# Kernel tuning notes

Hardware: AMD Instinct MI355X
Metric: run time of the kernel (lower is better)

## Reference

```python
import jax, jax.numpy as jnp
import numpy as np

E = 1024
H = 16
HD = E // H  # 64


def setup_inputs() -> dict:
    key = jax.random.key(0)
    ks = jax.random.split(key, 5)
    x = jax.random.normal(ks[0], (2, 2048, E), dtype=jnp.float32)
    s = 1.0 / np.sqrt(E)
    W_qkv = jax.random.uniform(ks[1], (E, 3 * E), jnp.float32, -s, s)
    b_qkv = jax.random.uniform(ks[2], (3 * E,), jnp.float32, -s, s)
    W_out = jax.random.uniform(ks[3], (E, E), jnp.float32, -s, s)
    b_out = jax.random.uniform(ks[4], (E,), jnp.float32, -s, s)
    return {"x": x, "W_qkv": W_qkv, "b_qkv": b_qkv, "W_out": W_out, "b_out": b_out}


def reference(x, W_qkv, b_qkv, W_out, b_out):
    B, N, _ = x.shape
    scale = HD ** (-0.5)
    qkv = x @ W_qkv + b_qkv                         # [B, N, 3E]
    qkv = qkv.reshape(B, N, H, 3 * HD)              # torch layout: per-head 3*hd chunk
    qkv = qkv.transpose(0, 2, 1, 3)                 # [B, H, N, 3*hd]
    q, k, v = jnp.split(qkv, 3, axis=-1)            # each [B, H, N, hd]
    attn = jnp.einsum('bhqd,bhkd->bhqk', q, k) * scale
    attn = jax.nn.softmax(attn, axis=-1)            # dropout is identity in eval
    out = jnp.einsum('bhqk,bhkd->bhqd', attn, v)    # [B, H, N, hd]
    out = out.transpose(0, 2, 1, 3).reshape(B, N, E)
    return out @ W_out + b_out
```

## Files before the change

### kernel.cpp

```cpp
#include <hip/hip_runtime.h>


#define SEQ 2048
#define NH  16

typedef __attribute__((ext_vector_type(8))) short short8;
typedef __attribute__((ext_vector_type(4))) short short4v;
typedef __attribute__((ext_vector_type(4))) float floatx4;
typedef __attribute__((ext_vector_type(4))) _Float16 half4;
typedef __attribute__((ext_vector_type(8))) _Float16 half8;
typedef __attribute__((ext_vector_type(2))) _Float16 half2v;
typedef __attribute__((ext_vector_type(2))) __fp16 fp16x2;

#define QSCALE 0.1803368801111204f

__device__ __forceinline__ short f2bf(float f) {
    union { float f; unsigned u; } v; v.f = f;
    unsigned r = v.u + 0x7fffu + ((v.u >> 16) & 1u);
    return (short)(r >> 16);
}

__device__ __forceinline__ float fast_exp2(float x) {
#if __has_builtin(__builtin_amdgcn_exp2f)
    return __builtin_amdgcn_exp2f(x);
#else
    return exp2f(x);
#endif
}

__device__ __forceinline__ half2v cvt_pk(float a, float b) {
#if __has_builtin(__builtin_amdgcn_cvt_pkrtz)
    union { fp16x2 i; half2v o; } u;
    u.i = __builtin_amdgcn_cvt_pkrtz(a, b);
    return u.o;
#else
    half2v r; r.x = (_Float16)a; r.y = (_Float16)b; return r;
#endif
}

#define GLDS16(gp, lp)                                                          \
    __builtin_amdgcn_global_load_lds(                                           \
        (const __attribute__((address_space(1))) unsigned int*)(gp),            \
        (__attribute__((address_space(3))) unsigned int*)(lp), 16, 0, 0)

__global__ __launch_bounds__(256) void prep_kernel(
    const float* __restrict__ x,  short* __restrict__ xb,
    const float* __restrict__ wq, short* __restrict__ wqkvt,
    const float* __restrict__ wo, short* __restrict__ woutt)
{
    const int tid = threadIdx.x;
    const int b = blockIdx.x;
    if (b < 2048) {
        int i = b * 256 + tid;
        const float4* in4 = (const float4*)x + (size_t)i * 2;
        float4 a = in4[0], c = in4[1];
        short8 o = { f2bf(a.x), f2bf(a.y), f2bf(a.z), f2bf(a.w),
                     f2bf(c.x), f2bf(c.y), f2bf(c.z), f2bf(c.w) };
        *((short8*)xb + i) = o;
        return;
    }
    __shared__ float T[64][65];
    const float* in; short* out; int R, C, c0, r0;
    if (b < 2816) {
        int t = b - 2048; in = wq; out = wqkvt; R = 1024; C = 3072;
        c0 = (t % 48) * 64; r0 = (t / 48) * 64;
    } else {
        int t = b - 2816; in = wo; out = woutt; R = 1024; C = 1024;
        c0 = (t & 15) * 64; r0 = (t >> 4) * 64;
    }
#pragma unroll
    for (int it = 0; it < 4; ++it) {
        int r = it * 16 + (tid >> 4), c = (tid & 15) * 4;
        float4 v = *(const float4*)(in + (size_t)(r0 + r) * C + c0 + c);
        T[c+0][r] = v.x; T[c+1][r] = v.y; T[c+2][r] = v.z; T[c+3][r] = v.w;
    }
    __syncthreads();
#pragma unroll
    for (int it = 0; it < 4; ++it) {
        int oc = it * 16 + (tid >> 4), k = (tid & 15) * 4;
        short4v o = { f2bf(T[oc][k]), f2bf(T[oc][k+1]), f2bf(T[oc][k+2]), f2bf(T[oc][k+3]) };
        *(short4v*)(out + (size_t)(c0 + oc) * R + r0 + k) = o;
    }
}

__global__ __launch_bounds__(256) void vtrans_kernel(
    const _Float16* __restrict__ vn, _Float16* __restrict__ vt)
{
    __shared__ _Float16 T[64][72];
    const int tid = threadIdx.x;
    const int bh = blockIdx.y, n0 = blockIdx.x * 64;
#pragma unroll
    for (int it = 0; it < 2; ++it) {
        int n = it * 32 + (tid >> 3), c = (tid & 7) * 8;
        const _Float16* p = vn + ((size_t)bh * SEQ + n0 + n) * 64 + c;
        half4 a = *(const half4*)(p);
        half4 b = *(const half4*)(p + 4);
        T[c+0][n] = a.x; T[c+1][n] = a.y; T[c+2][n] = a.z; T[c+3][n] = a.w;
        T[c+4][n] = b.x; T[c+5][n] = b.y; T[c+6][n] = b.z; T[c+7][n] = b.w;
    }
    __syncthreads();
#pragma unroll
    for (int it = 0; it < 2; ++it) {
        int idx = it * 256 + tid;
        int quad = idx & 3, d = (idx >> 2) & 63, u = idx >> 8;
        const _Float16* row = &T[d][u * 32 + quad * 4];
        half4 lo = *(const half4*)(row);
        half4 hi = *(const half4*)(row + 16);
        _Float16* q = vt + ((size_t)bh * 64 + d) * SEQ + n0 + u * 32 + quad * 8;
        *(half4*)(q)     = lo;
        *(half4*)(q + 4) = hi;
    }
}

#define GEMM_CORE(A_PTR, B_PTR, LDA, LDB)                                        \
    __shared__ short As[128 * 32];                                               \
    __shared__ short Bs[128 * 32];                                               \
    const int tid  = threadIdx.x;                                                \
    const int lane = tid & 63, w = tid >> 6;                                     \
    const int quad = lane >> 4, l16 = lane & 15;                                 \
    const int wm = w >> 1, wn = w & 1;                                           \
    const int c0 = blockIdx.x * 128, r0 = blockIdx.y * 128;                      \
    floatx4 acc[4][4];                                                           \
    _Pragma("unroll")                                                            \
    for (int i = 0; i < 4; ++i)                                                  \
        _Pragma("unroll")                                                        \
        for (int j = 0; j < 4; ++j) acc[i][j] = (floatx4){0.f, 0.f, 0.f, 0.f};   \
    const int srow = tid >> 2;                                                   \
    const int sgx  = ((tid & 3) ^ ((srow >> 1) & 3)) * 8;                        \
    const short* Ag = (A_PTR) + (size_t)(r0 + srow) * (LDA) + sgx;               \
    const short* Bg = (B_PTR) + (size_t)(c0 + srow) * (LDB) + sgx;               \
    const int fsw = (l16 >> 1) & 3;                                              \
    for (int kk = 0; kk < 1024; kk += 32) {                                      \
        __syncthreads();                                                         \
        GLDS16(Ag + kk,                      As + tid * 8);                      \
        GLDS16(Ag + (size_t)64 * (LDA) + kk, As + 2048 + tid * 8);               \
        GLDS16(Bg + kk,                      Bs + tid * 8);                      \
        GLDS16(Bg + (size_t)64 * (LDB) + kk, Bs + 2048 + tid * 8);               \
        __syncthreads();                                                         \
        short8 af[4], bf[4];                                                     \
        _Pragma("unroll")                                                        \
        for (int mt = 0; mt < 4; ++mt)                                           \
            af[mt] = *(const short8*)&As[(wm * 64 + mt * 16 + l16) * 32 + (quad ^ fsw) * 8]; \
        _Pragma("unroll")                                                        \
        for (int nt = 0; nt < 4; ++nt)                                           \
            bf[nt] = *(const short8*)&Bs[(wn * 64 + nt * 16 + l16) * 32 + (quad ^ fsw) * 8]; \
        _Pragma("unroll")                                                        \
        for (int mt = 0; mt < 4; ++mt)                                           \
            _Pragma("unroll")                                                    \
            for (int nt = 0; nt < 4; ++nt)                                       \
                acc[mt][nt] = __builtin_amdgcn_mfma_f32_16x16x32_bf16(           \
                    af[mt], bf[nt], acc[mt][nt], 0, 0, 0);                       \
    }

__global__ __launch_bounds__(256) void qkv_gemm_kernel(
    const short* __restrict__ wt, const short* __restrict__ xb,
    const float* __restrict__ bias,
    short* __restrict__ qb, short* __restrict__ kb, _Float16* __restrict__ vnb)
{
    GEMM_CORE(wt, xb, 1024, 1024)
#pragma unroll
    for (int mt = 0; mt < 4; ++mt) {
        int oc0 = r0 + wm * 64 + mt * 16 + quad * 4;
        int head = oc0 / 192;
        int t = (oc0 - head * 192) >> 6;
        int d0 = oc0 & 63;
        float4 bv = *(const float4*)(bias + oc0);
#pragma unroll
        for (int nt = 0; nt < 4; ++nt) {
            int tok = c0 + wn * 64 + nt * 16 + l16;
            int bh = (tok >> 11) * NH + head;
            size_t base = ((size_t)bh * SEQ + (tok & (SEQ - 1))) * 64 + d0;
            float v0 = acc[mt][nt][0] + bv.x, v1 = acc[mt][nt][1] + bv.y;
            float v2 = acc[mt][nt][2] + bv.z, v3 = acc[mt][nt][3] + bv.w;
            if (t == 0) {
                short4v o = { f2bf(v0 * QSCALE), f2bf(v1 * QSCALE),
                              f2bf(v2 * QSCALE), f2bf(v3 * QSCALE) };
                *(short4v*)(qb + base) = o;
            } else if (t == 1) {
                short4v o = { f2bf(v0), f2bf(v1), f2bf(v2), f2bf(v3) };
                *(short4v*)(kb + base) = o;
            } else {
                half4 o = { (_Float16)v0, (_Float16)v1, (_Float16)v2, (_Float16)v3 };
                *(half4*)(vnb + base) = o;
            }
        }
    }
}

__global__ __launch_bounds__(512) void out_gemm_kernel(
    const short* __restrict__ wt, const short* __restrict__ ab,
    const float* __restrict__ bias, float* __restrict__ out)
{
    __shared__ short As[128 * 32];
    __shared__ short Bs[128 * 32];
    const int tid  = threadIdx.x;
    const int lane = tid & 63, w = tid >> 6;
    const int quad = lane >> 4, l16 = lane & 15;
    const int wm = w >> 2, wn = w & 3;
    const int c0 = blockIdx.x * 128, r0 = blockIdx.y * 128;
    floatx4 acc[4][2];
#pragma unroll
    for (int i = 0; i < 4; ++i)
#pragma unroll
        for (int j = 0; j < 2; ++j) acc[i][j] = (floatx4){0.f, 0.f, 0.f, 0.f};
    const int srow = tid >> 2;
    const int sgx  = ((tid & 3) ^ ((srow >> 1) & 3)) * 8;
    const short* Ag = wt + (size_t)(r0 + srow) * 1024 + sgx;
    const short* Bg = ab + (size_t)(c0 + srow) * 1024 + sgx;
    const int fsw = (l16 >> 1) & 3;
    for (int kk = 0; kk < 1024; kk += 32) {
        __syncthreads();
        GLDS16(Ag + kk, As + tid * 8);
        GLDS16(Bg + kk, Bs + tid * 8);
        __syncthreads();
        short8 af[4], bf[2];
#pragma unroll
        for (int mt = 0; mt < 4; ++mt)
            af[mt] = *(const short8*)&As[(wm * 64 + mt * 16 + l16) * 32 + (quad ^ fsw) * 8];
#pragma unroll
        for (int nt = 0; nt < 2; ++nt)
            bf[nt] = *(const short8*)&Bs[(wn * 32 + nt * 16 + l16) * 32 + (quad ^ fsw) * 8];
#pragma unroll
        for (int mt = 0; mt < 4; ++mt)
#pragma unroll
            for (int nt = 0; nt < 2; ++nt)
                acc[mt][nt] = __builtin_amdgcn_mfma_f32_16x16x32_bf16(
                    af[mt], bf[nt], acc[mt][nt], 0, 0, 0);
    }
#pragma unroll
    for (int mt = 0; mt < 4; ++mt) {
        int oc0 = r0 + wm * 64 + mt * 16 + quad * 4;
        float4 bv = *(const float4*)(bias + oc0);
#pragma unroll
        for (int nt = 0; nt < 2; ++nt) {
            int tok = c0 + wn * 32 + nt * 16 + l16;
            float4 o = { acc[mt][nt][0] + bv.x, acc[mt][nt][1] + bv.y,
                         acc[mt][nt][2] + bv.z, acc[mt][nt][3] + bv.w };
            *(float4*)(out + (size_t)tok * 1024 + oc0) = o;
        }
    }
}

__global__ __launch_bounds__(256, 4) void attn_kernel(
    const short* __restrict__ qb, const short* __restrict__ kb,
    const _Float16* __restrict__ vtb, short* __restrict__ ob)
{
    __shared__ short    Ks[128 * 64];
    __shared__ _Float16 Vts[64 * 128];
    __shared__ float    Ls[4][32];
    const int tid  = threadIdx.x;
    const int lane = tid & 63, w = tid >> 6;
    const int quad = lane >> 4, l16 = lane & 15;
    const int qh = w >> 1, kq = w & 1;
    const int bh = blockIdx.y;
    const int q0 = blockIdx.x * 64;

    short8 aq[2][2];
#pragma unroll
    for (int qf = 0; qf < 2; ++qf) {
        const short* qp = qb + ((size_t)bh * SEQ + q0 + qh * 32 + qf * 16 + l16) * 64 + quad * 8;
        aq[qf][0] = *(const short8*)(qp);
        aq[qf][1] = *(const short8*)(qp + 32);
    }

    const int krow = tid >> 3, kg = tid & 7;
    const short* kgp = kb + ((size_t)bh * SEQ + krow) * 64 + (kg ^ (krow & 7)) * 8;
    const int vd = tid >> 2, vgg = tid & 3;
    const _Float16* vgp = vtb + ((size_t)bh * 64 + vd) * SEQ + (vgg ^ ((vd >> 1) & 3)) * 8;

    floatx4 o_acc[4][2];
#pragma unroll
    for (int dt = 0; dt < 4; ++dt)
#pragma unroll
        for (int qf = 0; qf < 2; ++qf) o_acc[dt][qf] = (floatx4){0.f, 0.f, 0.f, 0.f};
    float lw[2] = {0.f, 0.f};

    for (int k0 = 0; k0 < SEQ; k0 += 128) {
        __syncthreads();
        const short* kc_p = kgp + (size_t)k0 * 64;
        GLDS16(kc_p,        Ks + tid * 8);
        GLDS16(kc_p + 2048, Ks + 2048 + tid * 8);
        GLDS16(kc_p + 4096, Ks + 4096 + tid * 8);
        GLDS16(kc_p + 6144, Ks + 6144 + tid * 8);
        const _Float16* vc_p = vgp + k0;
        GLDS16((const short*)(vc_p),      (short*)Vts + tid * 8);
        GLDS16((const short*)(vc_p + 32), (short*)Vts + 2048 + tid * 8);
        GLDS16((const short*)(vc_p + 64), (short*)Vts + 4096 + tid * 8);
        GLDS16((const short*)(vc_p + 96), (short*)Vts + 6144 + tid * 8);
        __syncthreads();

#pragma unroll
        for (int uu = 0; uu < 2; ++uu) {
            const int u = kq * 2 + uu;
            half8 av8[4];
#pragma unroll
            for (int dt = 0; dt < 4; ++dt) {
                union { short8 s; half8 h; } vv;
                vv.s = *(const short8*)((const short*)Vts + u * 2048
                        + (dt * 16 + l16) * 32 + (quad ^ ((l16 >> 1) & 3)) * 8);
                av8[dt] = vv.h;
            }
            floatx4 sacc[2][2];
#pragma unroll
            for (int h = 0; h < 2; ++h) {
                const short* krp = &Ks[(u * 32 + h * 16 + l16) * 64];
                short8 ak0 = *(const short8*)(krp + ((0 + quad) ^ (l16 & 7)) * 8);
                short8 ak1 = *(const short8*)(krp + ((4 + quad) ^ (l16 & 7)) * 8);
#pragma unroll
                for (int qf = 0; qf < 2; ++qf) {
                    floatx4 z = (floatx4){0.f, 0.f, 0.f, 0.f};
                    z = __builtin_amdgcn_mfma_f32_16x16x32_bf16(ak0, aq[qf][0], z, 0, 0, 0);
                    sacc[h][qf] = __builtin_amdgcn_mfma_f32_16x16x32_bf16(ak1, aq[qf][1], z, 0, 0, 0);
                }
            }
            half8 pf8[2];
#pragma unroll
            for (int qf = 0; qf < 2; ++qf) {
                float p0 = fast_exp2(sacc[0][qf][0]);
                float p1 = fast_exp2(sacc[0][qf][1]);
                float p2 = fast_exp2(sacc[0][qf][2]);
                float p3 = fast_exp2(sacc[0][qf][3]);
                float p4 = fast_exp2(sacc[1][qf][0]);
                float p5 = fast_exp2(sacc[1][qf][1]);
                float p6 = fast_exp2(sacc[1][qf][2]);
                float p7 = fast_exp2(sacc[1][qf][3]);
                lw[qf] += ((p0 + p1) + (p2 + p3)) + ((p4 + p5) + (p6 + p7));
                half2v a = cvt_pk(p0, p1), b = cvt_pk(p2, p3);
                half2v c = cvt_pk(p4, p5), d = cvt_pk(p6, p7);
                pf8[qf] = (half8){a.x, a.y, b.x, b.y, c.x, c.y, d.x, d.y};
            }
#pragma unroll
            for (int dt = 0; dt < 4; ++dt)
#pragma unroll
                for (int qf = 0; qf < 2; ++qf)
                    o_acc[dt][qf] = __builtin_amdgcn_mfma_f32_16x16x32_f16(
                        av8[dt], pf8[qf], o_acc[dt][qf], 0, 0, 0);
        }
    }

#pragma unroll
    for (int qf = 0; qf < 2; ++qf) {
        lw[qf] += __shfl_xor(lw[qf], 16);
        lw[qf] += __shfl_xor(lw[qf], 32);
        if (quad == 0) Ls[w][qf * 16 + l16] = lw[qf];
    }

    float* Red = (float*)Ks;
    __syncthreads();
#pragma unroll
    for (int dt = 0; dt < 4; ++dt)
#pragma unroll
        for (int qf = 0; qf < 2; ++qf) {
            int fi = (((qh * 2 + qf) * 4 + dt) * 64 + lane) * 4;
            if (kq == 1) *(floatx4*)&Red[fi] = o_acc[dt][qf];
        }
    __syncthreads();
    if (kq == 0) {
        float inv[2];
#pragma unroll
        for (int qf = 0; qf < 2; ++qf) {
            int qi = qf * 16 + l16;
            inv[qf] = 1.0f / (Ls[qh * 2 + 0][qi] + Ls[qh * 2 + 1][qi]);
        }
        const int b = bh >> 4, h = bh & 15;
#pragma unroll
        for (int dt = 0; dt < 4; ++dt)
#pragma unroll
            for (int qf = 0; qf < 2; ++qf) {
                int fi = (((qh * 2 + qf) * 4 + dt) * 64 + lane) * 4;
                floatx4 o = o_acc[dt][qf] + *(const floatx4*)&Red[fi];
                int tok = b * SEQ + q0 + qh * 32 + qf * 16 + l16;
                short4v o4 = { f2bf(o[0] * inv[qf]), f2bf(o[1] * inv[qf]),
                               f2bf(o[2] * inv[qf]), f2bf(o[3] * inv[qf]) };
                *(short4v*)(ob + (size_t)tok * 1024 + h * 64 + dt * 16 + quad * 4) = o4;
            }
    }
}

extern "C" void kernel_launch(void* const* d_in, const int* in_sizes, int n_in,
                              void* d_out, int out_size, void* d_ws, size_t ws_size,
                              hipStream_t stream) {
    const float* x     = (const float*)d_in[0];
    const float* W_qkv = (const float*)d_in[1];
    const float* b_qkv = (const float*)d_in[2];
    const float* W_out = (const float*)d_in[3];
    const float* b_out = (const float*)d_in[4];
    float* out = (float*)d_out;

    short* xb      = (short*)d_ws;
    short* wqkvt   = xb    + (size_t)4096 * 1024;
    short* woutt   = wqkvt + (size_t)3072 * 1024;
    short* qb      = woutt + (size_t)1024 * 1024;
    short* kb      = qb    + (size_t)32 * SEQ * 64;
    _Float16* vnb  = (_Float16*)(kb + (size_t)32 * SEQ * 64);
    _Float16* vtb  = vnb + (size_t)32 * SEQ * 64;
    short* ob      = (short*)(vtb + (size_t)32 * 64 * SEQ);

    prep_kernel<<<3072, 256, 0, stream>>>(x, xb, W_qkv, wqkvt, W_out, woutt);
    qkv_gemm_kernel<<<dim3(32, 24), 256, 0, stream>>>(wqkvt, xb, b_qkv, qb, kb, vnb);
    vtrans_kernel<<<dim3(32, 32), 256, 0, stream>>>(vnb, vtb);
    attn_kernel<<<dim3(32, 32), 256, 0, stream>>>(qb, kb, vtb, ob);
    out_gemm_kernel<<<dim3(32, 8), 512, 0, stream>>>(woutt, ob, b_out, out);
}
```

Before: 194.4 us.

## Double-buffer K/V tiles in attention loop with 64-key chunks

Splits the shared K and V^T buffers into two 64-key halves and prefetches the next chunk via direct global-to-LDS loads while computing on the current one. This drops one of the two barriers per iteration and is meant to hide global load latency behind MFMA work. In exchange the iteration count doubles and each iteration does half the work per wave, so there is less compute per barrier. Correctness relies on the existing Red reuse of Ks still fitting, which should hold since total LDS size is unchanged.

```diff
diff --git a/kernel.cpp b/kernel.cpp
--- a/kernel.cpp
+++ b/kernel.cpp
@@ -245,8 +245,8 @@
     const short* __restrict__ qb, const short* __restrict__ kb,
     const _Float16* __restrict__ vtb, short* __restrict__ ob)
 {
-    __shared__ short    Ks[128 * 64];
-    __shared__ _Float16 Vts[64 * 128];
+    __shared__ short    Ks[2][64 * 64];
+    __shared__ _Float16 Vts[2][64 * 64];
     __shared__ float    Ls[4][32];
     const int tid  = threadIdx.x;
     const int lane = tid & 63, w = tid >> 6;
@@ -275,67 +275,72 @@
         for (int qf = 0; qf < 2; ++qf) o_acc[dt][qf] = (floatx4){0.f, 0.f, 0.f, 0.f};
     float lw[2] = {0.f, 0.f};
 
-    for (int k0 = 0; k0 < SEQ; k0 += 128) {
+    GLDS16(kgp,                        &Ks[0][0] + tid * 8);
+    GLDS16(kgp + 2048,                 &Ks[0][0] + 2048 + tid * 8);
+    GLDS16((const short*)(vgp),        (short*)&Vts[0][0] + tid * 8);
+    GLDS16((const short*)(vgp + 32),   (short*)&Vts[0][0] + 2048 + tid * 8);
+    __syncthreads();
+
+    int cur = 0;
+    for (int k0 = 0; k0 < SEQ; k0 += 64) {
+        if (k0 + 64 < SEQ) {
+            const short* kc_p = kgp + (size_t)(k0 + 64) * 64;
+            GLDS16(kc_p,        &Ks[cur ^ 1][0] + tid * 8);
+            GLDS16(kc_p + 2048, &Ks[cur ^ 1][0] + 2048 + tid * 8);
+            const _Float16* vc_p = vgp + (k0 + 64);
+            GLDS16((const short*)(vc_p),      (short*)&Vts[cur ^ 1][0] + tid * 8);
+            GLDS16((const short*)(vc_p + 32), (short*)&Vts[cur ^ 1][0] + 2048 + tid * 8);
+        }
+
+        const short* ksc = &Ks[cur][0];
+        const short* vsc = (const short*)&Vts[cur][0];
+        const int u = kq;
+        half8 av8[4];
+#pragma unroll
+        for (int dt = 0; dt < 4; ++dt) {
+            union { short8 s; half8 h; } vv;
+            vv.s = *(const short8*)(vsc + u * 2048
+                    + (dt * 16 + l16) * 32 + (quad ^ ((l16 >> 1) & 3)) * 8);
+            av8[dt] = vv.h;
+        }
+        floatx4 sacc[2][2];
+#pragma unroll
+        for (int h = 0; h < 2; ++h) {
+            const short* krp = ksc + (u * 32 + h * 16 + l16) * 64;
+            short8 ak0 = *(const short8*)(krp + ((0 + quad) ^ (l16 & 7)) * 8);
+            short8 ak1 = *(const short8*)(krp + ((4 + quad) ^ (l16 & 7)) * 8);
+#pragma unroll
+            for (int qf = 0; qf < 2; ++qf) {
+                floatx4 z = (floatx4){0.f, 0.f, 0.f, 0.f};
+                z = __builtin_amdgcn_mfma_f32_16x16x32_bf16(ak0, aq[qf][0], z, 0, 0, 0);
+                sacc[h][qf] = __builtin_amdgcn_mfma_f32_16x16x32_bf16(ak1, aq[qf][1], z, 0, 0, 0);
+            }
+        }
+        half8 pf8[2];
+#pragma unroll
+        for (int qf = 0; qf < 2; ++qf) {
+            float p0 = fast_exp2(sacc[0][qf][0]);
+            float p1 = fast_exp2(sacc[0][qf][1]);
+            float p2 = fast_exp2(sacc[0][qf][2]);
+            float p3 = fast_exp2(sacc[0][qf][3]);
+            float p4 = fast_exp2(sacc[1][qf][0]);
+            float p5 = fast_exp2(sacc[1][qf][1]);
+            float p6 = fast_exp2(sacc[1][qf][2]);
+            float p7 = fast_exp2(sacc[1][qf][3]);
+            lw[qf] += ((p0 + p1) + (p2 + p3)) + ((p4 + p5) + (p6 + p7));
+            half2v a = cvt_pk(p0, p1), b = cvt_pk(p2, p3);
+            half2v c = cvt_pk(p4, p5), d = cvt_pk(p6, p7);
+            pf8[qf] = (half8){a.x, a.y, b.x, b.y, c.x, c.y, d.x, d.y};
+        }
+#pragma unroll
+        for (int dt = 0; dt < 4; ++dt)
+#pragma unroll
+            for (int qf = 0; qf < 2; ++qf)
+                o_acc[dt][qf] = __builtin_amdgcn_mfma_f32_16x16x32_f16(
+                    av8[dt], pf8[qf], o_acc[dt][qf], 0, 0, 0);
+
         __syncthreads();
-        const short* kc_p = kgp + (size_t)k0 * 64;
-        GLDS16(kc_p,        Ks + tid * 8);
-        GLDS16(kc_p + 2048, Ks + 2048 + tid * 8);
-        GLDS16(kc_p + 4096, Ks + 4096 + tid * 8);
-        GLDS16(kc_p + 6144, Ks + 6144 + tid * 8);
-        const _Float16* vc_p = vgp + k0;
-        GLDS16((const short*)(vc_p),      (short*)Vts + tid * 8);
-        GLDS16((const short*)(vc_p + 32), (short*)Vts + 2048 + tid * 8);
-        GLDS16((const short*)(vc_p + 64), (short*)Vts + 4096 + tid * 8);
-        GLDS16((const short*)(vc_p + 96), (short*)Vts + 6144 + tid * 8);
-        __syncthreads();
-
-#pragma unroll
-        for (int uu = 0; uu < 2; ++uu) {
-            const int u = kq * 2 + uu;
-            half8 av8[4];
-#pragma unroll
-            for (int dt = 0; dt < 4; ++dt) {
-                union { short8 s; half8 h; } vv;
-                vv.s = *(const short8*)((const short*)Vts + u * 2048
-                        + (dt * 16 + l16) * 32 + (quad ^ ((l16 >> 1) & 3)) * 8);
-                av8[dt] = vv.h;
-            }
-            floatx4 sacc[2][2];
-#pragma unroll
-            for (int h = 0; h < 2; ++h) {
-                const short* krp = &Ks[(u * 32 + h * 16 + l16) * 64];
-                short8 ak0 = *(const short8*)(krp + ((0 + quad) ^ (l16 & 7)) * 8);
-                short8 ak1 = *(const short8*)(krp + ((4 + quad) ^ (l16 & 7)) * 8);
-#pragma unroll
-                for (int qf = 0; qf < 2; ++qf) {
-                    floatx4 z = (floatx4){0.f, 0.f, 0.f, 0.f};
-                    z = __builtin_amdgcn_mfma_f32_16x16x32_bf16(ak0, aq[qf][0], z, 0, 0, 0);
-                    sacc[h][qf] = __builtin_amdgcn_mfma_f32_16x16x32_bf16(ak1, aq[qf][1], z, 0, 0, 0);
-                }
-            }
-            half8 pf8[2];
-#pragma unroll
-            for (int qf = 0; qf < 2; ++qf) {
-                float p0 = fast_exp2(sacc[0][qf][0]);
-                float p1 = fast_exp2(sacc[0][qf][1]);
-                float p2 = fast_exp2(sacc[0][qf][2]);
-                float p3 = fast_exp2(sacc[0][qf][3]);
-                float p4 = fast_exp2(sacc[1][qf][0]);
-                float p5 = fast_exp2(sacc[1][qf][1]);
-                float p6 = fast_exp2(sacc[1][qf][2]);
-                float p7 = fast_exp2(sacc[1][qf][3]);
-                lw[qf] += ((p0 + p1) + (p2 + p3)) + ((p4 + p5) + (p6 + p7));
-                half2v a = cvt_pk(p0, p1), b = cvt_pk(p2, p3);
-                half2v c = cvt_pk(p4, p5), d = cvt_pk(p6, p7);
-                pf8[qf] = (half8){a.x, a.y, b.x, b.y, c.x, c.y, d.x, d.y};
-            }
-#pragma unroll
-            for (int dt = 0; dt < 4; ++dt)
-#pragma unroll
-                for (int qf = 0; qf < 2; ++qf)
-                    o_acc[dt][qf] = __builtin_amdgcn_mfma_f32_16x16x32_f16(
-                        av8[dt], pf8[qf], o_acc[dt][qf], 0, 0, 0);
-        }
+        cur ^= 1;
     }
 
 #pragma unroll
```

Result: faster. 190.0 us (-2.3%).
